# Performance work log

Hardware: AMD Instinct MI355X
Metric: run time of the kernel (lower is better)

Reference implementation:

```python
import jax
import jax.numpy as jnp
import numpy as np

LATENT = 4096
LABEL = 512
CLUSTERING_N = 1

# Sign with straight-through gradient (matches torch Sign.backward = identity)
@jax.custom_vjp
def sign_ste(x):
    return (x >= 0).astype(x.dtype) * 2 - 1

def _sign_fwd(x):
    return sign_ste(x), None

def _sign_bwd(_, g):
    return (g,)

sign_ste.defvjp(_sign_fwd, _sign_bwd)

# MaxOneHot: keep only argmax entry; backward passes 0.5*grad at argmax
@jax.custom_vjp
def max_onehot(x):
    idx = jnp.argmax(x)
    return jnp.zeros_like(x).at[idx].set(x[idx])

def _moh_fwd(x):
    idx = jnp.argmax(x)
    return jnp.zeros_like(x).at[idx].set(x[idx]), idx

def _moh_bwd(idx, g):
    return (0.5 * jnp.zeros_like(g).at[idx].set(g[idx]),)

max_onehot.defvjp(_moh_fwd, _moh_bwd)


def setup_inputs() -> dict:
    key = jax.random.key(0)
    k1, k2 = jax.random.split(key)
    s = jax.random.normal(k1, (LATENT,), dtype=jnp.float32)
    # matches torch init: 2*rand - 1 in (-1, 1)
    llv = 2.0 * jax.random.uniform(k2, (LABEL, LATENT), dtype=jnp.float32) - 1.0
    return {"s": s, "label_latent_vectors": llv}


def _hopfield_forward(s, llv):
    # weight build: x = sign(clamp(llv)); W = sum_i outer(x_i - rho) / label_size, zero diag
    x = sign_ste(jnp.clip(llv, -1.0, 1.0))          # [LABEL, LATENT]
    rho = jnp.mean(x)
    temp = x - rho                                   # [LABEL, LATENT]
    weight = (temp.T @ temp) / jnp.asarray(x.shape[0], x.dtype)  # [LATENT, LATENT]
    weight = weight - jnp.diag(jnp.diag(weight))

    # Gauss-Seidel sweep: sequential update s[i] = sign(W[i] . stop_grad(s))
    def step(s_carry, wi_i):
        wi, i = wi_i
        v = jnp.dot(wi, jax.lax.stop_gradient(s_carry))
        return s_carry.at[i].set(sign_ste(v)), None

    idxs = jnp.arange(weight.shape[0])
    for _ in range(CLUSTERING_N):
        s, _ = jax.lax.scan(step, s, (weight, idxs))

    scores = jnp.abs(s @ x.T) / jnp.asarray(s.shape[0], s.dtype)  # [LABEL]
    return max_onehot(scores)


def reference(s, label_latent_vectors):
    return _hopfield_forward(s, label_latent_vectors)
```

## Files before the change

kernel.cpp:

```cpp
#include <hip/hip_runtime.h>
#include <hip/hip_bf16.h>


#define OFF_COLB   0u
#define OFF_XBITS  (256u<<10)
#define OFF_XBW    (512u<<10)
#define OFF_KF     (768u<<10)
#define OFF_BCORR  (1792u<<10)
#define OFF_U      (1808u<<10)
#define OFF_CST    (1936u<<10)
#define OFF_P0     (2000u<<10)
#define OFF_HDR    (2019u<<10)
#define OFF_BS0    (2020u<<10)
#define OFF_BS0C   (2021u<<10)

template<int CTRL, int RMASK>
__device__ __forceinline__ float dpp_add(float x){
  int t = __builtin_amdgcn_update_dpp(0, __float_as_int(x), CTRL, RMASK, 0xf, true);
  return x + __int_as_float(t);
}
__device__ __forceinline__ float wave_allsum(float x){
  x = dpp_add<0x111,0xf>(x);
  x = dpp_add<0x112,0xf>(x);
  x = dpp_add<0x114,0xf>(x);
  x = dpp_add<0x118,0xf>(x);
  x = dpp_add<0x142,0xa>(x);
  x = dpp_add<0x143,0xc>(x);
  return __int_as_float(__builtin_amdgcn_readlane(__float_as_int(x), 63));
}

__global__ void k_xbp(const float* __restrict__ llv, const float* __restrict__ s0,
                      unsigned long long* __restrict__ xbits,
                      unsigned long long* __restrict__ xbitsW,
                      float* __restrict__ p0){
  int w = threadIdx.x >> 6, lane = threadIdx.x & 63;
  int l = blockIdx.x*4 + w;
  unsigned long long myword = 0;
  float acc = 0.0f;
  for (int c = 0; c < 64; ++c){
    float v = llv[(size_t)l*4096 + c*64 + lane];
    bool pos = (v >= 0.0f);
    unsigned long long b = __ballot(pos);
    if (c == lane) myword = b;
    float sg = pos ? 1.0f : -1.0f;
    acc = fmaf(sg, s0[c*64 + lane], acc);
  }
  xbits[(size_t)l*64 + lane] = myword;
  xbitsW[(size_t)lane*512 + l] = myword;
  float tot = wave_allsum(acc);
  if (lane == 0) p0[l] = tot;
}

__global__ void k_bitT(const unsigned long long* __restrict__ xbits,
                       unsigned long long* __restrict__ colbitsP){
  int li = blockIdx.x, ii = blockIdx.y, lane = threadIdx.x;
  unsigned long long w = xbits[(size_t)(li*64 + lane)*64 + ii];
  unsigned long long myw = 0;
  for (int j = 0; j < 64; ++j){
    unsigned long long b = __ballot((w >> j) & 1ull);
    if (j == lane) myw = b;
  }
  colbitsP[(size_t)li*4096 + ii*64 + lane] = myw;
}

__global__ __launch_bounds__(1024, 1)
void k_crc(const unsigned long long* __restrict__ colbitsP,
           const float* __restrict__ s0,
           float* __restrict__ hdr, float4* __restrict__ cst){
  __shared__ int cc[4096];
  __shared__ int red[1024];
  __shared__ float rhosh;
  int tid = threadIdx.x;
  int part = 0;
  #pragma unroll
  for (int k = 0; k < 4; ++k){
    int i = tid*4 + k;
    int c = 0;
    #pragma unroll
    for (int wl = 0; wl < 8; ++wl) c += __popcll(colbitsP[(size_t)wl*4096 + i]);
    cc[i] = c;
    part += c;
  }
  red[tid] = part;
  __syncthreads();
  for (int st = 512; st > 0; st >>= 1){
    if (tid < st) red[tid] += red[tid + st];
    __syncthreads();
  }
  if (tid == 0){
    int num = 2*red[0] - 2097152;
    float r = (float)num * (1.0f/2097152.0f);
    hdr[0] = r; rhosh = r;
  }
  __syncthreads();
  float rho = rhosh;
  #pragma unroll
  for (int k = 0; k < 4; ++k){
    int i = tid*4 + k;
    float c  = (float)(2*cc[i] - 512);
    float r2 = rho*rho;
    float q  = 512.0f + 512.0f*r2 - 2.0f*rho*c;
    float s  = s0[i];
    float4 o;
    o.x = q * s;
    o.y = rho*c - 512.0f*r2;
    o.z = 1.0f - s;
    o.w = c;
    cst[i] = o;
  }
}

__global__ __launch_bounds__(512, 1)
void k_kdu(const unsigned long long* __restrict__ colbitsP,
           const unsigned long long* __restrict__ xbits,
           const float4* __restrict__ cst, const float* __restrict__ s0,
           const float* __restrict__ hdr,
           float* __restrict__ Kf, float* __restrict__ baseCorr,
           float* __restrict__ blkS0, float* __restrict__ blkS0C,
           float* __restrict__ U){
  __shared__ unsigned long long cb[8][64];
  __shared__ float Kl[64][64];
  __shared__ float cs[64], ss[64];
  int b = blockIdx.x, i0 = b*64, tid = threadIdx.x;
  if (tid < 512) cb[tid>>6][tid&63] = colbitsP[(size_t)(tid>>6)*4096 + i0 + (tid&63)];
  if (tid < 64){ cs[tid] = cst[i0+tid].w; ss[tid] = s0[i0+tid]; }
  __syncthreads();
  float rho = hdr[0];
  float r2t = 512.0f*rho*rho;
  #pragma unroll
  for (int k = 0; k < 8; ++k){
    int q = tid*8 + k;
    int t = q >> 6, j = q & 63;
    int acc = 0;
    #pragma unroll
    for (int wl = 0; wl < 8; ++wl) acc += __popcll(cb[wl][t] ^ cb[wl][j]);
    float G = (float)(512 - 2*acc);
    float kf = G - rho*(cs[t]+cs[j]) + r2t;
    Kl[t][j] = kf;
    Kf[(size_t)b*4096 + q] = kf;
  }
  {
    int l = tid;
    unsigned long long w = xbits[(size_t)l*64 + b];
    unsigned int lo = (unsigned)w, hi = (unsigned)(w >> 32);
    unsigned int nlo = ~lo, nhi = ~hi;
    float acc = 0.0f;
    #pragma unroll
    for (int j = 0; j < 32; ++j){
      unsigned int m = (nlo << (31-j)) & 0x80000000u;
      acc += __uint_as_float(__float_as_uint(ss[j]) ^ m);
    }
    #pragma unroll
    for (int j = 0; j < 32; ++j){
      unsigned int m = (nhi << (31-j)) & 0x80000000u;
      acc += __uint_as_float(__float_as_uint(ss[32+j]) ^ m);
    }
    U[(size_t)b*512 + l] = acc;
  }
  __syncthreads();
  if (tid < 64){
    float bc = 0.0f;
    for (int j = 0; j < tid; ++j) bc = fmaf(ss[j], Kl[tid][j], bc);
    baseCorr[i0 + tid] = bc;
  }
  if (tid == 64){
    float a = 0.0f, b2 = 0.0f;
    for (int j = 0; j < 64; ++j){ a += ss[j]; b2 = fmaf(ss[j], cs[j], b2); }
    blkS0[b] = a; blkS0C[b] = b2;
  }
}

#define ACCX(A, F, W, JS) { \
  unsigned int m_ = ((~(W)) << (31-(JS))) & 0x80000000u; \
  A += __uint_as_float(__float_as_uint(F) ^ m_); }
#define ACCQ(A, F, W, JS) { float4 q_ = pw[F]; \
  ACCX(A, q_.x, W, (JS)+0) ACCX(A, q_.y, W, (JS)+1) \
  ACCX(A, q_.z, W, (JS)+2) ACCX(A, q_.w, W, (JS)+3) }

#define BSTP(KVAL, J) { \
  unsigned long long neg_ = __ballot(__float_as_int(v) < 0); \
  unsigned b_ = (unsigned)(neg_ >> (J)) & 1u; \
  sg_ |= ((unsigned long long)(b_ ^ 1u)) << (J); \
  v = v + __uint_as_float(__float_as_uint(KVAL) ^ (b_ << 31)); }
#define BST4(Q, J0) BSTP(Q.x,(J0)+0) BSTP(Q.y,(J0)+1) BSTP(Q.z,(J0)+2) BSTP(Q.w,(J0)+3)

__global__ __launch_bounds__(512, 1)
void k_sweep6(const unsigned long long* __restrict__ colbitsP,
              const unsigned long long* __restrict__ xbitsW,
              const unsigned long long* __restrict__ xbits,
              const float* __restrict__ Kf, const float* __restrict__ baseCorr,
              const float* __restrict__ blkS0, const float* __restrict__ blkS0C,
              const float* __restrict__ U, const float4* __restrict__ cst,
              const float* __restrict__ p0, const float* __restrict__ s0,
              const float* __restrict__ hdr, float* __restrict__ out)
{
  __shared__ float Kl[2][64][64];
  __shared__ unsigned long long cbl[2][8][64];
  __shared__ unsigned long long xbl[2][512];
  __shared__ float Ul[2][512];
  __shared__ float4 cstl[2][64];
  __shared__ float bcl[2][64];
  __shared__ float bs0l[64], bscl[64];
  __shared__ float p[512];
  __shared__ float part[8][64];
  __shared__ float red[512];
  __shared__ unsigned long long sig;
  __shared__ unsigned long long sbl[64];
  __shared__ int bestkey;

  int tid = threadIdx.x, g = tid >> 6, t = tid & 63;
  float rho = hdr[0];

  p[tid] = p0[tid];
  red[tid] = p0[tid];
  if (tid < 64){ bs0l[tid] = blkS0[tid]; bscl[tid] = blkS0C[tid]; }
  if (tid == 0) bestkey = -1;
  __syncthreads();
  for (int st = 256; st > 0; st >>= 1){ if (tid < st) red[tid] += red[tid+st]; __syncthreads(); }
  float Preg = red[0];
  __syncthreads();
  { float a = 0.0f; for (int k = 0; k < 8; ++k) a += s0[tid*8 + k]; red[tid] = a; }
  __syncthreads();
  for (int st = 256; st > 0; st >>= 1){ if (tid < st) red[tid] += red[tid+st]; __syncthreads(); }
  float Treg = red[0];
  __syncthreads();

  {
    const float4* Ks = (const float4*)(Kf);
    #pragma unroll
    for (int k = 0; k < 4; ++k){
      int e = tid + k*512;
      float4 vv = Ks[e];
      int gie = e >> 10, row = (e >> 4) & 63, f = e & 15;
      *((float4*)&Kl[gie][row][0] + (f ^ (row & 15))) = vv;
    }
    #pragma unroll
    for (int k = 0; k < 2; ++k){
      int e = tid + k*512;
      int run = e >> 6, tt = e & 63, gie = run >> 3, wl = run & 7;
      cbl[gie][wl][tt] = colbitsP[(size_t)wl*4096 + gie*64 + tt];
    }
    #pragma unroll
    for (int k = 0; k < 2; ++k){
      int e = tid + k*512;
      ((unsigned long long*)xbl)[e] = xbitsW[e];
    }
    #pragma unroll
    for (int k = 0; k < 2; ++k){
      int e = tid + k*512;
      ((float*)Ul)[e] = U[e];
    }
    if (tid < 128){
      ((float4*)cstl)[tid] = cst[tid];
      ((float*)bcl)[tid]   = baseCorr[tid];
    }
  }
  __syncthreads();

  for (int grp = 0; grp < 32; ++grp){
    int ng = grp + 1;
    bool pf = (ng < 32);
    float4 kv0, kv1, kv2, kv3, cstv;
    unsigned long long cbv0, cbv1, xbv0, xbv1;
    float uv0, uv1, bcv;
    if (pf){
      const float4* Ks = (const float4*)(Kf + (size_t)ng*8192);
      kv0 = Ks[tid]; kv1 = Ks[tid+512]; kv2 = Ks[tid+1024]; kv3 = Ks[tid+1536];
      { int e = tid;       int run = e>>6, tt = e&63;
        cbv0 = colbitsP[(size_t)(run&7)*4096 + (ng*2 + (run>>3))*64 + tt]; }
      { int e = tid + 512; int run = e>>6, tt = e&63;
        cbv1 = colbitsP[(size_t)(run&7)*4096 + (ng*2 + (run>>3))*64 + tt]; }
      xbv0 = xbitsW[(size_t)ng*1024 + tid]; xbv1 = xbitsW[(size_t)ng*1024 + tid + 512];
      uv0  = U[(size_t)ng*1024 + tid];      uv1  = U[(size_t)ng*1024 + tid + 512];
      if (tid < 128){ cstv = cst[ng*128 + tid]; bcv = baseCorr[ng*128 + tid]; }
    }

    #pragma unroll
    for (int gi = 0; gi < 2; ++gi){
      int b = grp*2 + gi;
      {
        unsigned long long w = cbl[gi][g][t];
        unsigned int lo = (unsigned)w, hi = (unsigned)(w >> 32);
        const float4* pw = (const float4*)(p + g*64);
        float a0 = 0.0f, a1 = 0.0f, a2 = 0.0f, a3 = 0.0f;
        ACCQ(a0, 0,  lo, 0)  ACCQ(a0, 1,  lo, 4)  ACCQ(a0, 2,  lo, 8)  ACCQ(a0, 3,  lo, 12)
        ACCQ(a1, 4,  lo, 16) ACCQ(a1, 5,  lo, 20) ACCQ(a1, 6,  lo, 24) ACCQ(a1, 7,  lo, 28)
        ACCQ(a2, 8,  hi, 0)  ACCQ(a2, 9,  hi, 4)  ACCQ(a2, 10, hi, 8)  ACCQ(a2, 11, hi, 12)
        ACCQ(a3, 12, hi, 16) ACCQ(a3, 13, hi, 20) ACCQ(a3, 14, hi, 24) ACCQ(a3, 15, hi, 28)
        part[g][t] = (a0 + a1) + (a2 + a3);
      }
      __syncthreads();

      unsigned long long sg_ = 0ull;
      float4 cc = make_float4(0.f,0.f,0.f,0.f);
      if (g == 0){
        const float4* Kp = (const float4*)&Kl[gi][t][0];
        int sw = t & 15;
        float S = 0.0f;
        #pragma unroll
        for (int gg = 0; gg < 8; ++gg) S += part[gg][t];
        cc = cstl[gi][t];
        float bc_ = bcl[gi][t];
        float v = S - cc.x - rho*Preg - cc.y*Treg - bc_;
        float4 C0 = Kp[0^sw], C1 = Kp[1^sw], C2 = Kp[2^sw];
        BST4(C0, 0);   C0 = Kp[3^sw];
        BST4(C1, 4);   C1 = Kp[4^sw];
        BST4(C2, 8);   C2 = Kp[5^sw];
        BST4(C0, 12);  C0 = Kp[6^sw];
        BST4(C1, 16);  C1 = Kp[7^sw];
        BST4(C2, 20);  C2 = Kp[8^sw];
        BST4(C0, 24);  C0 = Kp[9^sw];
        BST4(C1, 28);  C1 = Kp[10^sw];
        BST4(C2, 32);  C2 = Kp[11^sw];
        BST4(C0, 36);  C0 = Kp[12^sw];
        BST4(C1, 40);  C1 = Kp[13^sw];
        BST4(C2, 44);  C2 = Kp[14^sw];
        BST4(C0, 48);  C0 = Kp[15^sw];
        BST4(C1, 52);
        BST4(C2, 56);
        BST4(C0, 60);
        if (t == 0){ sig = sg_; sbl[b] = sg_; }
      }
      __syncthreads();
      if (g == 0){
        float sv = ((sg_ >> t) & 1ull) ? cc.w : -cc.w;
        float sc = wave_allsum(sv);
        int pcs = __popcll(sg_);
        Preg += sc - bscl[b];
        Treg += (float)(2*pcs - 64) - bs0l[b];
      }
      {
        unsigned long long sgv = sig;
        int pc = __popcll(xbl[gi][tid] ^ sgv);
        p[tid] = p[tid] + (float)(64 - 2*pc) - Ul[gi][tid];
      }
    }

    __syncthreads();
    if (pf){
      { int e = tid;        int gie=e>>10, row=(e>>4)&63, f=e&15;
        *((float4*)&Kl[gie][row][0] + (f ^ (row & 15))) = kv0; }
      { int e = tid + 512;  int gie=e>>10, row=(e>>4)&63, f=e&15;
        *((float4*)&Kl[gie][row][0] + (f ^ (row & 15))) = kv1; }
      { int e = tid + 1024; int gie=e>>10, row=(e>>4)&63, f=e&15;
        *((float4*)&Kl[gie][row][0] + (f ^ (row & 15))) = kv2; }
      { int e = tid + 1536; int gie=e>>10, row=(e>>4)&63, f=e&15;
        *((float4*)&Kl[gie][row][0] + (f ^ (row & 15))) = kv3; }
      { int e = tid;       int run=e>>6, tt=e&63; cbl[run>>3][run&7][tt] = cbv0; }
      { int e = tid + 512; int run=e>>6, tt=e&63; cbl[run>>3][run&7][tt] = cbv1; }
      ((unsigned long long*)xbl)[tid]       = xbv0;
      ((unsigned long long*)xbl)[tid + 512] = xbv1;
      ((float*)Ul)[tid]       = uv0;
      ((float*)Ul)[tid + 512] = uv1;
      if (tid < 128){ ((float4*)cstl)[tid] = cstv; ((float*)bcl)[tid] = bcv; }
    }
    __syncthreads();
  }

  {
    int acc = 0;
    #pragma unroll
    for (int w = 0; w < 64; ++w)
      acc += __popcll(xbits[(size_t)tid*64 + w] ^ sbl[w]);
    int dot = 4096 - 2*acc;
    int ad  = dot < 0 ? -dot : dot;
    int key = (ad << 10) | (511 - tid);
    atomicMax(&bestkey, key);
    __syncthreads();
    int bl = 511 - (bestkey & 1023);
    float val = (float)(bestkey >> 10) * (1.0f/4096.0f);
    out[tid] = (tid == bl) ? val : 0.0f;
  }
}

extern "C" void kernel_launch(void* const* d_in, const int* in_sizes, int n_in,
                              void* d_out, int out_size, void* d_ws, size_t ws_size,
                              hipStream_t stream){
  const float* s0  = (const float*)d_in[0];
  const float* llv = (const float*)d_in[1];
  float* out = (float*)d_out;
  char* ws = (char*)d_ws;

  unsigned long long* colbitsP = (unsigned long long*)(ws + OFF_COLB);
  unsigned long long* xbits    = (unsigned long long*)(ws + OFF_XBITS);
  unsigned long long* xbitsW   = (unsigned long long*)(ws + OFF_XBW);
  float*  Kf    = (float*)(ws + OFF_KF);
  float*  bcorr = (float*)(ws + OFF_BCORR);
  float*  U     = (float*)(ws + OFF_U);
  float4* cst   = (float4*)(ws + OFF_CST);
  float*  p0    = (float*)(ws + OFF_P0);
  float*  hdr   = (float*)(ws + OFF_HDR);
  float*  bS0   = (float*)(ws + OFF_BS0);
  float*  bS0C  = (float*)(ws + OFF_BS0C);

  k_xbp<<<128, 256, 0, stream>>>(llv, s0, xbits, xbitsW, p0);
  k_bitT<<<dim3(8, 64), 64, 0, stream>>>(xbits, colbitsP);
  k_crc<<<1, 1024, 0, stream>>>(colbitsP, s0, hdr, cst);
  k_kdu<<<64, 512, 0, stream>>>(colbitsP, xbits, cst, s0, hdr, Kf, bcorr, bS0, bS0C, U);
  k_sweep6<<<1, 512, 0, stream>>>(colbitsP, xbitsW, xbits, Kf, bcorr, bS0, bS0C, U, cst, p0, s0, hdr, out);
}
```

Before: 202.4 us.

## Fuse bit transpose and column-count stats into the K-build kernel

Removes the separate bit-transpose and single-block column-count kernels. The global positive count is accumulated by atomic adds in the first kernel and rho is derived from it downstream. Each K-build block now transposes its own column slice and computes its per-column constants locally. This cuts two launches and a serial single-block reduction, at the cost of an added memset and atomics.

```diff
diff --git a/kernel.cpp b/kernel.cpp
--- a/kernel.cpp
+++ b/kernel.cpp
@@ -32,7 +32,7 @@
 __global__ void k_xbp(const float* __restrict__ llv, const float* __restrict__ s0,
                       unsigned long long* __restrict__ xbits,
                       unsigned long long* __restrict__ xbitsW,
-                      float* __restrict__ p0){
+                      float* __restrict__ p0, int* __restrict__ totpos){
   int w = threadIdx.x >> 6, lane = threadIdx.x & 63;
   int l = blockIdx.x*4 + w;
   unsigned long long myword = 0;
@@ -49,72 +49,14 @@
   xbitsW[(size_t)lane*512 + l] = myword;
   float tot = wave_allsum(acc);
   if (lane == 0) p0[l] = tot;
-}
-
-__global__ void k_bitT(const unsigned long long* __restrict__ xbits,
-                       unsigned long long* __restrict__ colbitsP){
-  int li = blockIdx.x, ii = blockIdx.y, lane = threadIdx.x;
-  unsigned long long w = xbits[(size_t)(li*64 + lane)*64 + ii];
-  unsigned long long myw = 0;
-  for (int j = 0; j < 64; ++j){
-    unsigned long long b = __ballot((w >> j) & 1ull);
-    if (j == lane) myw = b;
-  }
-  colbitsP[(size_t)li*4096 + ii*64 + lane] = myw;
-}
-
-__global__ __launch_bounds__(1024, 1)
-void k_crc(const unsigned long long* __restrict__ colbitsP,
+  float tp = wave_allsum((float)__popcll(myword));
+  if (lane == 0) atomicAdd(totpos, (int)tp);
+}
+
+__global__ __launch_bounds__(512, 1)
+void k_kdu(const unsigned long long* __restrict__ xbits, const int* __restrict__ totpos,
            const float* __restrict__ s0,
-           float* __restrict__ hdr, float4* __restrict__ cst){
-  __shared__ int cc[4096];
-  __shared__ int red[1024];
-  __shared__ float rhosh;
-  int tid = threadIdx.x;
-  int part = 0;
-  #pragma unroll
-  for (int k = 0; k < 4; ++k){
-    int i = tid*4 + k;
-    int c = 0;
-    #pragma unroll
-    for (int wl = 0; wl < 8; ++wl) c += __popcll(colbitsP[(size_t)wl*4096 + i]);
-    cc[i] = c;
-    part += c;
-  }
-  red[tid] = part;
-  __syncthreads();
-  for (int st = 512; st > 0; st >>= 1){
-    if (tid < st) red[tid] += red[tid + st];
-    __syncthreads();
-  }
-  if (tid == 0){
-    int num = 2*red[0] - 2097152;
-    float r = (float)num * (1.0f/2097152.0f);
-    hdr[0] = r; rhosh = r;
-  }
-  __syncthreads();
-  float rho = rhosh;
-  #pragma unroll
-  for (int k = 0; k < 4; ++k){
-    int i = tid*4 + k;
-    float c  = (float)(2*cc[i] - 512);
-    float r2 = rho*rho;
-    float q  = 512.0f + 512.0f*r2 - 2.0f*rho*c;
-    float s  = s0[i];
-    float4 o;
-    o.x = q * s;
-    o.y = rho*c - 512.0f*r2;
-    o.z = 1.0f - s;
-    o.w = c;
-    cst[i] = o;
-  }
-}
-
-__global__ __launch_bounds__(512, 1)
-void k_kdu(const unsigned long long* __restrict__ colbitsP,
-           const unsigned long long* __restrict__ xbits,
-           const float4* __restrict__ cst, const float* __restrict__ s0,
-           const float* __restrict__ hdr,
+           unsigned long long* __restrict__ colbitsP, float4* __restrict__ cst,
            float* __restrict__ Kf, float* __restrict__ baseCorr,
            float* __restrict__ blkS0, float* __restrict__ blkS0C,
            float* __restrict__ U){
@@ -122,10 +64,39 @@
   __shared__ float Kl[64][64];
   __shared__ float cs[64], ss[64];
   int b = blockIdx.x, i0 = b*64, tid = threadIdx.x;
-  if (tid < 512) cb[tid>>6][tid&63] = colbitsP[(size_t)(tid>>6)*4096 + i0 + (tid&63)];
-  if (tid < 64){ cs[tid] = cst[i0+tid].w; ss[tid] = s0[i0+tid]; }
-  __syncthreads();
-  float rho = hdr[0];
+  int g = tid >> 6, lane = tid & 63;
+
+  unsigned long long word = xbits[(size_t)(g*64 + lane)*64 + b];
+  unsigned long long myw = 0;
+  for (int t = 0; t < 64; ++t){
+    unsigned long long bl = __ballot((word >> t) & 1ull);
+    if (t == lane) myw = bl;
+  }
+  cb[g][lane] = myw;
+  colbitsP[(size_t)g*4096 + i0 + lane] = myw;
+  if (tid < 64) ss[tid] = s0[i0 + tid];
+  __syncthreads();
+
+  int num = 2*totpos[0] - 2097152;
+  float rho = (float)num * (1.0f/2097152.0f);
+  if (tid < 64){
+    int ccnt = 0;
+    #pragma unroll
+    for (int wl = 0; wl < 8; ++wl) ccnt += __popcll(cb[wl][tid]);
+    float c = (float)(2*ccnt - 512);
+    cs[tid] = c;
+    float r2 = rho*rho;
+    float q  = 512.0f + 512.0f*r2 - 2.0f*rho*c;
+    float sv = ss[tid];
+    float4 o;
+    o.x = q * sv;
+    o.y = rho*c - 512.0f*r2;
+    o.z = 1.0f - sv;
+    o.w = c;
+    cst[i0 + tid] = o;
+  }
+  __syncthreads();
+
   float r2t = 512.0f*rho*rho;
   #pragma unroll
   for (int k = 0; k < 8; ++k){
@@ -192,7 +163,7 @@
               const float* __restrict__ blkS0, const float* __restrict__ blkS0C,
               const float* __restrict__ U, const float4* __restrict__ cst,
               const float* __restrict__ p0, const float* __restrict__ s0,
-              const float* __restrict__ hdr, float* __restrict__ out)
+              const int* __restrict__ totpos, float* __restrict__ out)
 {
   __shared__ float Kl[2][64][64];
   __shared__ unsigned long long cbl[2][8][64];
@@ -209,7 +180,8 @@
   __shared__ int bestkey;
 
   int tid = threadIdx.x, g = tid >> 6, t = tid & 63;
-  float rho = hdr[0];
+  int num = 2*totpos[0] - 2097152;
+  float rho = (float)num * (1.0f/2097152.0f);
 
   p[tid] = p0[tid];
   red[tid] = p0[tid];
@@ -389,13 +361,12 @@
   float*  U     = (float*)(ws + OFF_U);
   float4* cst   = (float4*)(ws + OFF_CST);
   float*  p0    = (float*)(ws + OFF_P0);
-  float*  hdr   = (float*)(ws + OFF_HDR);
+  int*    cnt   = (int*)(ws + OFF_HDR);
   float*  bS0   = (float*)(ws + OFF_BS0);
   float*  bS0C  = (float*)(ws + OFF_BS0C);
 
-  k_xbp<<<128, 256, 0, stream>>>(llv, s0, xbits, xbitsW, p0);
-  k_bitT<<<dim3(8, 64), 64, 0, stream>>>(xbits, colbitsP);
-  k_crc<<<1, 1024, 0, stream>>>(colbitsP, s0, hdr, cst);
-  k_kdu<<<64, 512, 0, stream>>>(colbitsP, xbits, cst, s0, hdr, Kf, bcorr, bS0, bS0C, U);
-  k_sweep6<<<1, 512, 0, stream>>>(colbitsP, xbitsW, xbits, Kf, bcorr, bS0, bS0C, U, cst, p0, s0, hdr, out);
-}
+  hipMemsetAsync(cnt, 0, sizeof(int), stream);
+  k_xbp<<<128, 256, 0, stream>>>(llv, s0, xbits, xbitsW, p0, cnt);
+  k_kdu<<<64, 512, 0, stream>>>(xbits, cnt, s0, colbitsP, cst, Kf, bcorr, bS0, bS0C, U);
+  k_sweep6<<<1, 512, 0, stream>>>(colbitsP, xbitsW, xbits, Kf, bcorr, bS0, bS0C, U, cst, p0, s0, cnt, out);
+}
```

Result: no change. 202.6 us (+0.1%).
